# Kernel optimization log

Measured on AMD Instinct MI355X. Metric: run time of the kernel, lower is better.

Reference implementation:

```python
import jax, jax.numpy as jnp
import numpy as np

N = 50000   # nodes
E = 640000  # edges
IN = 128
HID = 128
EPS = 1e-5


def setup_inputs() -> dict:
    key = jax.random.key(0)
    ks = jax.random.split(key, 8)
    s = 1.0 / np.sqrt(IN)
    inp = {
        "x": jax.random.normal(ks[0], (N, IN), jnp.float32),
        "src": jax.random.randint(ks[1], (E,), 0, N, dtype=jnp.int32),
        "dst": jax.random.randint(ks[2], (E,), 0, N, dtype=jnp.int32),
        "W1": jax.random.normal(ks[3], (IN, HID), jnp.float32) * s,
        "b1": jnp.zeros((HID,), jnp.float32),
        "g1": jnp.ones((HID,), jnp.float32),
        "be1": jnp.zeros((HID,), jnp.float32),
        "W2": jax.random.normal(ks[4], (HID, HID), jnp.float32) * s,
        "b2": jnp.zeros((HID,), jnp.float32),
        "g2": jnp.ones((HID,), jnp.float32),
        "be2": jnp.zeros((HID,), jnp.float32),
        "W3": jax.random.normal(ks[5], (HID, HID), jnp.float32) * s,
        "b3": jnp.zeros((HID,), jnp.float32),
        "g3": jnp.ones((HID,), jnp.float32),
        "be3": jnp.zeros((HID,), jnp.float32),
    }
    return inp


def _layernorm(h, g, b):
    mu = jnp.mean(h, axis=-1, keepdims=True)
    var = jnp.mean(jnp.square(h - mu), axis=-1, keepdims=True)
    return g * (h - mu) * jax.lax.rsqrt(var + EPS) + b


def _gcn_conv(h, W, b, src, dst):
    # Kipf & Welling GCN: D^{-1/2} (A + I) D^{-1/2} (H W) + b
    # self-loops added with weight 1; degree computed on the target index.
    hw = h @ W                                          # [N, HID]
    deg = jax.ops.segment_sum(jnp.ones((E,), h.dtype), dst, num_segments=N) + 1.0
    dinv = jax.lax.rsqrt(deg)                           # deg >= 1 due to self loop
    msg = hw[src] * (dinv[src] * dinv[dst])[:, None]    # gather + normalize, [E, HID]
    agg = jax.ops.segment_sum(msg, dst, num_segments=N)  # scatter-add
    agg = agg + hw * (dinv * dinv)[:, None]             # self-loop contribution
    return agg + b


def reference(x, src, dst, W1, b1, g1, be1, W2, b2, g2, be2, W3, b3, g3, be3):
    layers = [(W1, b1, g1, be1), (W2, b2, g2, be2), (W3, b3, g3, be3)]
    h = x
    for i, (W, b, g, be) in enumerate(layers):
        h_in = h
        h = _gcn_conv(h, W, b, src, dst)
        h = _layernorm(h, g, be)
        h = jax.nn.relu(h)
        # dropout: eval mode -> identity
        if i > 0 and h.shape == h_in.shape:
            h = h + h_in
    return h
```

## Files before the change

kernel.cpp:

```cpp
#include <hip/hip_runtime.h>
#include <hip/hip_bf16.h>

#define NFEAT 128
#define EPSLN 1e-5f
#define PAD 64

typedef __attribute__((ext_vector_type(8))) short short8;
typedef __attribute__((ext_vector_type(4))) float f32x4;

__device__ __forceinline__ float bf2f(ushort u) {
    union { uint u32; float f; } v; v.u32 = ((uint)u) << 16; return v.f;
}
__device__ __forceinline__ ushort f2bf(float f) {
    union { float f; uint u32; } v; v.f = f;
    uint u = v.u32;
    u += 0x7FFF + ((u >> 16) & 1);
    return (ushort)(u >> 16);
}

__global__ void setup_kernel(int4* __restrict__ cnt4, int ncnt4,
                             const float* __restrict__ W0, const float* __restrict__ W1,
                             const float* __restrict__ W2,
                             ushort* __restrict__ Wt0, ushort* __restrict__ Wt1,
                             ushort* __restrict__ Wt2) {
    int i = blockIdx.x * 256 + threadIdx.x;
    if (i < ncnt4) cnt4[i] = make_int4(0, 0, 0, 0);
    if (i < 3 * NFEAT * NFEAT) {
        int l = i / (NFEAT * NFEAT);
        int r = i - l * (NFEAT * NFEAT);
        int k = r >> 7, n = r & 127;
        const float* W = (l == 0) ? W0 : (l == 1) ? W1 : W2;
        ushort* Wt = (l == 0) ? Wt0 : (l == 1) ? Wt1 : Wt2;
        Wt[n * NFEAT + k] = f2bf(W[r]);
    }
}

__global__ void fill_kernel(const int* __restrict__ src, const int* __restrict__ dst,
                            int* __restrict__ cnt, int* __restrict__ csr, int E) {
    int e = blockIdx.x * 256 + threadIdx.x;
    if (e < E) {
        int d = dst[e];
        int s = src[e];
        int pos = atomicAdd(&cnt[d], 1);
        if (pos < PAD) csr[d * PAD + pos] = s;
    }
}

__global__ __launch_bounds__(256) void gemm_mfma_kernel(const ushort* __restrict__ hb,
                                                        const float* __restrict__ hf,
                                                        const ushort* __restrict__ Wt,
                                                        const int* __restrict__ cnt,
                                                        ushort* __restrict__ hw, int N) {
    __shared__ ushort WtL[NFEAT * NFEAT];
    {
        const uint4* src4 = (const uint4*)Wt;
        uint4* dst4 = (uint4*)WtL;
        #pragma unroll
        for (int i = 0; i < 8; ++i)
            dst4[threadIdx.x + i * 256] = src4[threadIdx.x + i * 256];
    }
    __syncthreads();

    const int wave = threadIdx.x >> 6;
    const int lane = threadIdx.x & 63;
    const int quad = lane >> 4;
    const int l16  = lane & 15;
    const int row0 = blockIdx.x * 128 + wave * 32;

    short8 afrag[2][4];
    #pragma unroll
    for (int t = 0; t < 2; ++t) {
        const int arow = row0 + t * 16 + l16;
        const bool rowok = (arow < N);
        if (hf) {
            const float4* fp = (const float4*)(hf + (size_t)arow * NFEAT);
            #pragma unroll
            for (int ks = 0; ks < 4; ++ks) {
                short8 a = short8{0, 0, 0, 0, 0, 0, 0, 0};
                if (rowok) {
                    float4 u0 = fp[ks * 8 + quad * 2];
                    float4 u1 = fp[ks * 8 + quad * 2 + 1];
                    a[0] = (short)f2bf(u0.x); a[1] = (short)f2bf(u0.y);
                    a[2] = (short)f2bf(u0.z); a[3] = (short)f2bf(u0.w);
                    a[4] = (short)f2bf(u1.x); a[5] = (short)f2bf(u1.y);
                    a[6] = (short)f2bf(u1.z); a[7] = (short)f2bf(u1.w);
                }
                afrag[t][ks] = a;
            }
        } else {
            const short8* ap = (const short8*)(hb + (size_t)arow * NFEAT);
            #pragma unroll
            for (int ks = 0; ks < 4; ++ks) {
                if (rowok) afrag[t][ks] = ap[ks * 4 + quad];
                else       afrag[t][ks] = short8{0, 0, 0, 0, 0, 0, 0, 0};
            }
        }
    }

    f32x4 acc[2][8];
    #pragma unroll
    for (int t = 0; t < 2; ++t)
        #pragma unroll
        for (int ct = 0; ct < 8; ++ct) acc[t][ct] = f32x4{0.f, 0.f, 0.f, 0.f};

    #pragma unroll
    for (int ct = 0; ct < 8; ++ct) {
        const int bcol = ct * 16 + l16;
        const short8* bp = (const short8*)(WtL + (size_t)bcol * NFEAT);
        #pragma unroll
        for (int ks = 0; ks < 4; ++ks) {
            short8 bfrag = bp[ks * 4 + quad];
            acc[0][ct] = __builtin_amdgcn_mfma_f32_16x16x32_bf16(afrag[0][ks], bfrag, acc[0][ct], 0, 0, 0);
            acc[1][ct] = __builtin_amdgcn_mfma_f32_16x16x32_bf16(afrag[1][ks], bfrag, acc[1][ct], 0, 0, 0);
        }
    }

    #pragma unroll
    for (int t = 0; t < 2; ++t) {
        const int orow_base = row0 + t * 16 + quad * 4;
        #pragma unroll
        for (int r = 0; r < 4; ++r) {
            const int orow = orow_base + r;
            if (orow < N) {
                const float di = rsqrtf((float)cnt[orow] + 1.0f);
                ushort* op = hw + (size_t)orow * NFEAT + l16;
                #pragma unroll
                for (int ct = 0; ct < 8; ++ct)
                    op[ct * 16] = f2bf(acc[t][ct][r] * di);
            }
        }
    }
}

__global__ __launch_bounds__(256) void agg_ln_kernel(const ushort* __restrict__ hwb,
                                                     const int* __restrict__ cnt,
                                                     const int* __restrict__ csr,
                                                     const float* __restrict__ bias,
                                                     const float* __restrict__ gamma,
                                                     const float* __restrict__ beta,
                                                     const ushort* __restrict__ hres_b,
                                                     float* __restrict__ outf,
                                                     ushort* __restrict__ outb,
                                                     int N) {
    const int node = blockIdx.x * 4 + (threadIdx.x >> 6);
    const int lane = threadIdx.x & 63;
    if (node >= N) return;
    const int quad = lane >> 4;
    const int l16  = lane & 15;
    const int c0i  = l16 * 8;

    const int cn  = cnt[node];
    const int deg = (cn < PAD) ? cn : PAD;
    const float di = rsqrtf((float)cn + 1.0f);
    const int* ce = csr + (size_t)node * PAD;
    const uint4* hw4 = (const uint4*)hwb;

    int myidx = 0;
    if (lane < deg) myidx = ce[lane];

    uint4 hv = hw4[(size_t)node * 16 + l16];

    float acc[8];
    #pragma unroll
    for (int i = 0; i < 8; ++i) acc[i] = 0.f;

    const int ng = (deg + 15) >> 4;
    for (int gi = 0; gi < ng; ++gi) {
        const int jb = gi * 16 + quad;
        const int s0 = __shfl(myidx, jb);
        const int s1 = __shfl(myidx, jb + 4);
        const int s2 = __shfl(myidx, jb + 8);
        const int s3 = __shfl(myidx, jb + 12);
        const float w0 = (jb      < deg) ? 1.f : 0.f;
        const float w1 = (jb + 4  < deg) ? 1.f : 0.f;
        const float w2 = (jb + 8  < deg) ? 1.f : 0.f;
        const float w3 = (jb + 12 < deg) ? 1.f : 0.f;
        uint4 v0 = hw4[(size_t)s0 * 16 + l16];
        uint4 v1 = hw4[(size_t)s1 * 16 + l16];
        uint4 v2 = hw4[(size_t)s2 * 16 + l16];
        uint4 v3 = hw4[(size_t)s3 * 16 + l16];
        acc[0] = fmaf(bf2f((ushort)(v0.x & 0xFFFF)), w0, acc[0]);
        acc[1] = fmaf(bf2f((ushort)(v0.x >> 16)),   w0, acc[1]);
        acc[2] = fmaf(bf2f((ushort)(v0.y & 0xFFFF)), w0, acc[2]);
        acc[3] = fmaf(bf2f((ushort)(v0.y >> 16)),   w0, acc[3]);
        acc[4] = fmaf(bf2f((ushort)(v0.z & 0xFFFF)), w0, acc[4]);
        acc[5] = fmaf(bf2f((ushort)(v0.z >> 16)),   w0, acc[5]);
        acc[6] = fmaf(bf2f((ushort)(v0.w & 0xFFFF)), w0, acc[6]);
        acc[7] = fmaf(bf2f((ushort)(v0.w >> 16)),   w0, acc[7]);
        acc[0] = fmaf(bf2f((ushort)(v1.x & 0xFFFF)), w1, acc[0]);
        acc[1] = fmaf(bf2f((ushort)(v1.x >> 16)),   w1, acc[1]);
        acc[2] = fmaf(bf2f((ushort)(v1.y & 0xFFFF)), w1, acc[2]);
        acc[3] = fmaf(bf2f((ushort)(v1.y >> 16)),   w1, acc[3]);
        acc[4] = fmaf(bf2f((ushort)(v1.z & 0xFFFF)), w1, acc[4]);
        acc[5] = fmaf(bf2f((ushort)(v1.z >> 16)),   w1, acc[5]);
        acc[6] = fmaf(bf2f((ushort)(v1.w & 0xFFFF)), w1, acc[6]);
        acc[7] = fmaf(bf2f((ushort)(v1.w >> 16)),   w1, acc[7]);
        acc[0] = fmaf(bf2f((ushort)(v2.x & 0xFFFF)), w2, acc[0]);
        acc[1] = fmaf(bf2f((ushort)(v2.x >> 16)),   w2, acc[1]);
        acc[2] = fmaf(bf2f((ushort)(v2.y & 0xFFFF)), w2, acc[2]);
        acc[3] = fmaf(bf2f((ushort)(v2.y >> 16)),   w2, acc[3]);
        acc[4] = fmaf(bf2f((ushort)(v2.z & 0xFFFF)), w2, acc[4]);
        acc[5] = fmaf(bf2f((ushort)(v2.z >> 16)),   w2, acc[5]);
        acc[6] = fmaf(bf2f((ushort)(v2.w & 0xFFFF)), w2, acc[6]);
        acc[7] = fmaf(bf2f((ushort)(v2.w >> 16)),   w2, acc[7]);
        acc[0] = fmaf(bf2f((ushort)(v3.x & 0xFFFF)), w3, acc[0]);
        acc[1] = fmaf(bf2f((ushort)(v3.x >> 16)),   w3, acc[1]);
        acc[2] = fmaf(bf2f((ushort)(v3.y & 0xFFFF)), w3, acc[2]);
        acc[3] = fmaf(bf2f((ushort)(v3.y >> 16)),   w3, acc[3]);
        acc[4] = fmaf(bf2f((ushort)(v3.z & 0xFFFF)), w3, acc[4]);
        acc[5] = fmaf(bf2f((ushort)(v3.z >> 16)),   w3, acc[5]);
        acc[6] = fmaf(bf2f((ushort)(v3.w & 0xFFFF)), w3, acc[6]);
        acc[7] = fmaf(bf2f((ushort)(v3.w >> 16)),   w3, acc[7]);
    }

    #pragma unroll
    for (int i = 0; i < 8; ++i) {
        acc[i] += __shfl_xor(acc[i], 16);
        acc[i] += __shfl_xor(acc[i], 32);
    }

    float4 b0 = ((const float4*)(bias + c0i))[0];
    float4 b1 = ((const float4*)(bias + c0i))[1];
    float x[8];
    x[0] = (acc[0] + bf2f((ushort)(hv.x & 0xFFFF))) * di + b0.x;
    x[1] = (acc[1] + bf2f((ushort)(hv.x >> 16)))   * di + b0.y;
    x[2] = (acc[2] + bf2f((ushort)(hv.y & 0xFFFF))) * di + b0.z;
    x[3] = (acc[3] + bf2f((ushort)(hv.y >> 16)))   * di + b0.w;
    x[4] = (acc[4] + bf2f((ushort)(hv.z & 0xFFFF))) * di + b1.x;
    x[5] = (acc[5] + bf2f((ushort)(hv.z >> 16)))   * di + b1.y;
    x[6] = (acc[6] + bf2f((ushort)(hv.w & 0xFFFF))) * di + b1.z;
    x[7] = (acc[7] + bf2f((ushort)(hv.w >> 16)))   * di + b1.w;

    float s = 0.f, sq = 0.f;
    #pragma unroll
    for (int i = 0; i < 8; ++i) { s += x[i]; sq += x[i] * x[i]; }
    #pragma unroll
    for (int o = 8; o > 0; o >>= 1) {
        s  += __shfl_xor(s, o);
        sq += __shfl_xor(sq, o);
    }
    const float mu  = s * (1.0f / NFEAT);
    const float var = sq * (1.0f / NFEAT) - mu * mu;
    const float rs  = rsqrtf(var + EPSLN);

    float4 g0 = ((const float4*)(gamma + c0i))[0];
    float4 g1 = ((const float4*)(gamma + c0i))[1];
    float4 e0 = ((const float4*)(beta + c0i))[0];
    float4 e1 = ((const float4*)(beta + c0i))[1];
    float gm[8] = {g0.x, g0.y, g0.z, g0.w, g1.x, g1.y, g1.z, g1.w};
    float bt[8] = {e0.x, e0.y, e0.z, e0.w, e1.x, e1.y, e1.z, e1.w};

    float y[8];
    #pragma unroll
    for (int i = 0; i < 8; ++i)
        y[i] = fmaxf(gm[i] * (x[i] - mu) * rs + bt[i], 0.0f);

    if (hres_b) {
        uint4 hr = ((const uint4*)hres_b)[(size_t)node * 16 + l16];
        y[0] += bf2f((ushort)(hr.x & 0xFFFF));
        y[1] += bf2f((ushort)(hr.x >> 16));
        y[2] += bf2f((ushort)(hr.y & 0xFFFF));
        y[3] += bf2f((ushort)(hr.y >> 16));
        y[4] += bf2f((ushort)(hr.z & 0xFFFF));
        y[5] += bf2f((ushort)(hr.z >> 16));
        y[6] += bf2f((ushort)(hr.w & 0xFFFF));
        y[7] += bf2f((ushort)(hr.w >> 16));
    }

    if (quad == 0) {
        if (outf) {
            float4* op = (float4*)(outf + (size_t)node * NFEAT + c0i);
            op[0] = make_float4(y[0], y[1], y[2], y[3]);
            op[1] = make_float4(y[4], y[5], y[6], y[7]);
        }
        if (outb) {
            uint4 ob;
            ob.x = (uint)f2bf(y[0]) | ((uint)f2bf(y[1]) << 16);
            ob.y = (uint)f2bf(y[2]) | ((uint)f2bf(y[3]) << 16);
            ob.z = (uint)f2bf(y[4]) | ((uint)f2bf(y[5]) << 16);
            ob.w = (uint)f2bf(y[6]) | ((uint)f2bf(y[7]) << 16);
            ((uint4*)outb)[(size_t)node * 16 + l16] = ob;
        }
    }
}

extern "C" void kernel_launch(void* const* d_in, const int* in_sizes, int n_in,
                              void* d_out, int out_size, void* d_ws, size_t ws_size,
                              hipStream_t stream) {
    const float* x   = (const float*)d_in[0];
    const int*   src = (const int*)d_in[1];
    const int*   dst = (const int*)d_in[2];
    const float* W[3]  = {(const float*)d_in[3], (const float*)d_in[7],  (const float*)d_in[11]};
    const float* b[3]  = {(const float*)d_in[4], (const float*)d_in[8],  (const float*)d_in[12]};
    const float* g[3]  = {(const float*)d_in[5], (const float*)d_in[9],  (const float*)d_in[13]};
    const float* be[3] = {(const float*)d_in[6], (const float*)d_in[10], (const float*)d_in[14]};

    const int N = in_sizes[0] / NFEAT;
    const int E = in_sizes[1];

    char* ws = (char*)d_ws;
    size_t off = 0;
    auto carve = [&](size_t bytes) -> char* {
        char* p = ws + off;
        off = (off + bytes + 255) & ~(size_t)255;
        return p;
    };
    const int ncnt4 = (N + 3) / 4;
    int*    cnt = (int*)   carve((size_t)ncnt4 * 4 * sizeof(int));
    int*    csr = (int*)   carve(((size_t)N * PAD + 64) * sizeof(int));
    ushort* hwb = (ushort*)carve((size_t)N * NFEAT * sizeof(ushort));
    ushort* h1b = (ushort*)carve((size_t)N * NFEAT * sizeof(ushort));
    ushort* h2b = (ushort*)carve((size_t)N * NFEAT * sizeof(ushort));
    ushort* Wt[3];
    for (int l = 0; l < 3; ++l) Wt[l] = (ushort*)carve(NFEAT * NFEAT * sizeof(ushort));
    (void)ws_size;

    int setup_threads = 3 * NFEAT * NFEAT;
    if (ncnt4 > setup_threads) setup_threads = ncnt4;
    setup_kernel<<<(setup_threads + 255) / 256, 256, 0, stream>>>(
        (int4*)cnt, ncnt4, W[0], W[1], W[2], Wt[0], Wt[1], Wt[2]);

    fill_kernel<<<(E + 255) / 256, 256, 0, stream>>>(src, dst, cnt, csr, E);

    const ushort* hbin[3]  = {nullptr, h1b, h2b};
    const float*  hfin[3]  = {x, nullptr, nullptr};
    const ushort* hresb[3] = {nullptr, h1b, h2b};
    float*        houtf[3] = {nullptr, nullptr, (float*)d_out};
    ushort*       houtb[3] = {h1b, h2b, nullptr};

    const int gemm_blocks = (N + 127) / 128;
    const int agg_blocks = (N + 3) / 4;

    for (int l = 0; l < 3; ++l) {
        gemm_mfma_kernel<<<gemm_blocks, 256, 0, stream>>>(hbin[l], hfin[l], Wt[l], cnt, hwb, N);
        agg_ln_kernel<<<agg_blocks, 256, 0, stream>>>(hwb, cnt, csr,
                                                      b[l], g[l], be[l],
                                                      hresb[l], houtf[l], houtb[l], N);
    }
}
```

Baseline: 270.3 us.

## Stage GEMM output through LDS for coalesced stores; use zero pad row in aggregation

The GEMM epilogue now writes scaled bf16 results into shared memory (reusing the weight tile buffer after a barrier), then emits full-row 16-byte coalesced global stores instead of strided 2-byte stores. The aggregation kernel replaces masked FMAs with plain adds by pointing out-of-range neighbor slots at an extra zeroed row N of the hw buffer. This removes scattered narrow writes and per-element multiply masking, at the cost of an extra sync, LDS traffic, and redundant gathers of the pad row.

```diff
diff --git a/kernel.cpp b/kernel.cpp
--- a/kernel.cpp
+++ b/kernel.cpp
@@ -19,12 +19,14 @@
 }
 
 __global__ void setup_kernel(int4* __restrict__ cnt4, int ncnt4,
+                             ushort* __restrict__ hwb_padrow,
                              const float* __restrict__ W0, const float* __restrict__ W1,
                              const float* __restrict__ W2,
                              ushort* __restrict__ Wt0, ushort* __restrict__ Wt1,
                              ushort* __restrict__ Wt2) {
     int i = blockIdx.x * 256 + threadIdx.x;
     if (i < ncnt4) cnt4[i] = make_int4(0, 0, 0, 0);
+    if (i < 16) ((uint4*)hwb_padrow)[i] = make_uint4(0, 0, 0, 0);
     if (i < 3 * NFEAT * NFEAT) {
         int l = i / (NFEAT * NFEAT);
         int r = i - l * (NFEAT * NFEAT);
@@ -115,20 +117,30 @@
         }
     }
 
+    __syncthreads();
+    ushort* tb = WtL + wave * (32 * NFEAT);
+
     #pragma unroll
     for (int t = 0; t < 2; ++t) {
-        const int orow_base = row0 + t * 16 + quad * 4;
         #pragma unroll
         for (int r = 0; r < 4; ++r) {
-            const int orow = orow_base + r;
-            if (orow < N) {
-                const float di = rsqrtf((float)cnt[orow] + 1.0f);
-                ushort* op = hw + (size_t)orow * NFEAT + l16;
-                #pragma unroll
-                for (int ct = 0; ct < 8; ++ct)
-                    op[ct * 16] = f2bf(acc[t][ct][r] * di);
-            }
-        }
+            const int rl = t * 16 + quad * 4 + r;
+            const int orow = row0 + rl;
+            const float di = (orow < N) ? rsqrtf((float)cnt[orow] + 1.0f) : 0.f;
+            #pragma unroll
+            for (int ct = 0; ct < 8; ++ct)
+                tb[rl * NFEAT + ct * 16 + l16] = f2bf(acc[t][ct][r] * di);
+        }
+    }
+    #pragma unroll
+    for (int i = 0; i < 8; ++i) {
+        const int c = i * 64 + lane;
+        const int rl = c >> 4;
+        const int ch = c & 15;
+        const int orow = row0 + rl;
+        uint4 v = *(const uint4*)(tb + rl * NFEAT + ch * 8);
+        if (orow < N)
+            ((uint4*)(hw + (size_t)orow * NFEAT))[ch] = v;
     }
 }
 
@@ -155,9 +167,7 @@
     const int* ce = csr + (size_t)node * PAD;
     const uint4* hw4 = (const uint4*)hwb;
 
-    int myidx = 0;
-    if (lane < deg) myidx = ce[lane];
-
+    int myidx = (lane < deg) ? ce[lane] : N;
     uint4 hv = hw4[(size_t)node * 16 + l16];
 
     float acc[8];
@@ -171,46 +181,26 @@
         const int s1 = __shfl(myidx, jb + 4);
         const int s2 = __shfl(myidx, jb + 8);
         const int s3 = __shfl(myidx, jb + 12);
-        const float w0 = (jb      < deg) ? 1.f : 0.f;
-        const float w1 = (jb + 4  < deg) ? 1.f : 0.f;
-        const float w2 = (jb + 8  < deg) ? 1.f : 0.f;
-        const float w3 = (jb + 12 < deg) ? 1.f : 0.f;
         uint4 v0 = hw4[(size_t)s0 * 16 + l16];
         uint4 v1 = hw4[(size_t)s1 * 16 + l16];
         uint4 v2 = hw4[(size_t)s2 * 16 + l16];
         uint4 v3 = hw4[(size_t)s3 * 16 + l16];
-        acc[0] = fmaf(bf2f((ushort)(v0.x & 0xFFFF)), w0, acc[0]);
-        acc[1] = fmaf(bf2f((ushort)(v0.x >> 16)),   w0, acc[1]);
-        acc[2] = fmaf(bf2f((ushort)(v0.y & 0xFFFF)), w0, acc[2]);
-        acc[3] = fmaf(bf2f((ushort)(v0.y >> 16)),   w0, acc[3]);
-        acc[4] = fmaf(bf2f((ushort)(v0.z & 0xFFFF)), w0, acc[4]);
-        acc[5] = fmaf(bf2f((ushort)(v0.z >> 16)),   w0, acc[5]);
-        acc[6] = fmaf(bf2f((ushort)(v0.w & 0xFFFF)), w0, acc[6]);
-        acc[7] = fmaf(bf2f((ushort)(v0.w >> 16)),   w0, acc[7]);
-        acc[0] = fmaf(bf2f((ushort)(v1.x & 0xFFFF)), w1, acc[0]);
-        acc[1] = fmaf(bf2f((ushort)(v1.x >> 16)),   w1, acc[1]);
-        acc[2] = fmaf(bf2f((ushort)(v1.y & 0xFFFF)), w1, acc[2]);
-        acc[3] = fmaf(bf2f((ushort)(v1.y >> 16)),   w1, acc[3]);
-        acc[4] = fmaf(bf2f((ushort)(v1.z & 0xFFFF)), w1, acc[4]);
-        acc[5] = fmaf(bf2f((ushort)(v1.z >> 16)),   w1, acc[5]);
-        acc[6] = fmaf(bf2f((ushort)(v1.w & 0xFFFF)), w1, acc[6]);
-        acc[7] = fmaf(bf2f((ushort)(v1.w >> 16)),   w1, acc[7]);
-        acc[0] = fmaf(bf2f((ushort)(v2.x & 0xFFFF)), w2, acc[0]);
-        acc[1] = fmaf(bf2f((ushort)(v2.x >> 16)),   w2, acc[1]);
-        acc[2] = fmaf(bf2f((ushort)(v2.y & 0xFFFF)), w2, acc[2]);
-        acc[3] = fmaf(bf2f((ushort)(v2.y >> 16)),   w2, acc[3]);
-        acc[4] = fmaf(bf2f((ushort)(v2.z & 0xFFFF)), w2, acc[4]);
-        acc[5] = fmaf(bf2f((ushort)(v2.z >> 16)),   w2, acc[5]);
-        acc[6] = fmaf(bf2f((ushort)(v2.w & 0xFFFF)), w2, acc[6]);
-        acc[7] = fmaf(bf2f((ushort)(v2.w >> 16)),   w2, acc[7]);
-        acc[0] = fmaf(bf2f((ushort)(v3.x & 0xFFFF)), w3, acc[0]);
-        acc[1] = fmaf(bf2f((ushort)(v3.x >> 16)),   w3, acc[1]);
-        acc[2] = fmaf(bf2f((ushort)(v3.y & 0xFFFF)), w3, acc[2]);
-        acc[3] = fmaf(bf2f((ushort)(v3.y >> 16)),   w3, acc[3]);
-        acc[4] = fmaf(bf2f((ushort)(v3.z & 0xFFFF)), w3, acc[4]);
-        acc[5] = fmaf(bf2f((ushort)(v3.z >> 16)),   w3, acc[5]);
-        acc[6] = fmaf(bf2f((ushort)(v3.w & 0xFFFF)), w3, acc[6]);
-        acc[7] = fmaf(bf2f((ushort)(v3.w >> 16)),   w3, acc[7]);
+        acc[0] += bf2f((ushort)(v0.x & 0xFFFF)) + bf2f((ushort)(v1.x & 0xFFFF))
+                + bf2f((ushort)(v2.x & 0xFFFF)) + bf2f((ushort)(v3.x & 0xFFFF));
+        acc[1] += bf2f((ushort)(v0.x >> 16)) + bf2f((ushort)(v1.x >> 16))
+                + bf2f((ushort)(v2.x >> 16)) + bf2f((ushort)(v3.x >> 16));
+        acc[2] += bf2f((ushort)(v0.y & 0xFFFF)) + bf2f((ushort)(v1.y & 0xFFFF))
+                + bf2f((ushort)(v2.y & 0xFFFF)) + bf2f((ushort)(v3.y & 0xFFFF));
+        acc[3] += bf2f((ushort)(v0.y >> 16)) + bf2f((ushort)(v1.y >> 16))
+                + bf2f((ushort)(v2.y >> 16)) + bf2f((ushort)(v3.y >> 16));
+        acc[4] += bf2f((ushort)(v0.z & 0xFFFF)) + bf2f((ushort)(v1.z & 0xFFFF))
+                + bf2f((ushort)(v2.z & 0xFFFF)) + bf2f((ushort)(v3.z & 0xFFFF));
+        acc[5] += bf2f((ushort)(v0.z >> 16)) + bf2f((ushort)(v1.z >> 16))
+                + bf2f((ushort)(v2.z >> 16)) + bf2f((ushort)(v3.z >> 16));
+        acc[6] += bf2f((ushort)(v0.w & 0xFFFF)) + bf2f((ushort)(v1.w & 0xFFFF))
+                + bf2f((ushort)(v2.w & 0xFFFF)) + bf2f((ushort)(v3.w & 0xFFFF));
+        acc[7] += bf2f((ushort)(v0.w >> 16)) + bf2f((ushort)(v1.w >> 16))
+                + bf2f((ushort)(v2.w >> 16)) + bf2f((ushort)(v3.w >> 16));
     }
 
     #pragma unroll
@@ -221,19 +211,19 @@
 
     float4 b0 = ((const float4*)(bias + c0i))[0];
     float4 b1 = ((const float4*)(bias + c0i))[1];
-    float x[8];
-    x[0] = (acc[0] + bf2f((ushort)(hv.x & 0xFFFF))) * di + b0.x;
-    x[1] = (acc[1] + bf2f((ushort)(hv.x >> 16)))   * di + b0.y;
-    x[2] = (acc[2] + bf2f((ushort)(hv.y & 0xFFFF))) * di + b0.z;
-    x[3] = (acc[3] + bf2f((ushort)(hv.y >> 16)))   * di + b0.w;
-    x[4] = (acc[4] + bf2f((ushort)(hv.z & 0xFFFF))) * di + b1.x;
-    x[5] = (acc[5] + bf2f((ushort)(hv.z >> 16)))   * di + b1.y;
-    x[6] = (acc[6] + bf2f((ushort)(hv.w & 0xFFFF))) * di + b1.z;
-    x[7] = (acc[7] + bf2f((ushort)(hv.w >> 16)))   * di + b1.w;
+    float xv[8];
+    xv[0] = (acc[0] + bf2f((ushort)(hv.x & 0xFFFF))) * di + b0.x;
+    xv[1] = (acc[1] + bf2f((ushort)(hv.x >> 16)))   * di + b0.y;
+    xv[2] = (acc[2] + bf2f((ushort)(hv.y & 0xFFFF))) * di + b0.z;
+    xv[3] = (acc[3] + bf2f((ushort)(hv.y >> 16)))   * di + b0.w;
+    xv[4] = (acc[4] + bf2f((ushort)(hv.z & 0xFFFF))) * di + b1.x;
+    xv[5] = (acc[5] + bf2f((ushort)(hv.z >> 16)))   * di + b1.y;
+    xv[6] = (acc[6] + bf2f((ushort)(hv.w & 0xFFFF))) * di + b1.z;
+    xv[7] = (acc[7] + bf2f((ushort)(hv.w >> 16)))   * di + b1.w;
 
     float s = 0.f, sq = 0.f;
     #pragma unroll
-    for (int i = 0; i < 8; ++i) { s += x[i]; sq += x[i] * x[i]; }
+    for (int i = 0; i < 8; ++i) { s += xv[i]; sq += xv[i] * xv[i]; }
     #pragma unroll
     for (int o = 8; o > 0; o >>= 1) {
         s  += __shfl_xor(s, o);
@@ -253,7 +243,7 @@
     float y[8];
     #pragma unroll
     for (int i = 0; i < 8; ++i)
-        y[i] = fmaxf(gm[i] * (x[i] - mu) * rs + bt[i], 0.0f);
+        y[i] = fmaxf(gm[i] * (xv[i] - mu) * rs + bt[i], 0.0f);
 
     if (hres_b) {
         uint4 hr = ((const uint4*)hres_b)[(size_t)node * 16 + l16];
@@ -308,7 +298,7 @@
     const int ncnt4 = (N + 3) / 4;
     int*    cnt = (int*)   carve((size_t)ncnt4 * 4 * sizeof(int));
     int*    csr = (int*)   carve(((size_t)N * PAD + 64) * sizeof(int));
-    ushort* hwb = (ushort*)carve((size_t)N * NFEAT * sizeof(ushort));
+    ushort* hwb = (ushort*)carve((size_t)(N + 1) * NFEAT * sizeof(ushort));
     ushort* h1b = (ushort*)carve((size_t)N * NFEAT * sizeof(ushort));
     ushort* h2b = (ushort*)carve((size_t)N * NFEAT * sizeof(ushort));
     ushort* Wt[3];
@@ -318,7 +308,8 @@
     int setup_threads = 3 * NFEAT * NFEAT;
     if (ncnt4 > setup_threads) setup_threads = ncnt4;
     setup_kernel<<<(setup_threads + 255) / 256, 256, 0, stream>>>(
-        (int4*)cnt, ncnt4, W[0], W[1], W[2], Wt[0], Wt[1], Wt[2]);
+        (int4*)cnt, ncnt4, hwb + (size_t)N * NFEAT,
+        W[0], W[1], W[2], Wt[0], Wt[1], Wt[2]);
 
     fill_kernel<<<(E + 255) / 256, 256, 0, stream>>>(src, dst, cnt, csr, E);
 
```

Result: no change. 265.8 us (-1.7%).
